# Kernel tuning notes

Measured on AMD Instinct MI355X. Metric: run time of the kernel, lower is better.

## Reference

```python
import jax, jax.numpy as jnp
import numpy as np

GRID = (32, 32)
LATENT = 256
ALPHA = 1.0
DECAY = 0.9


def _cdist(a, b):
    # Euclidean pairwise distance with a grad-safe sqrt (0 where d2==0, like torch.cdist).
    d2 = jnp.sum(a * a, -1)[:, None] + jnp.sum(b * b, -1)[None, :] - 2.0 * (a @ b.T)
    d2 = jnp.maximum(d2, 0.0)
    mask = d2 > 0
    return jnp.where(mask, jnp.sqrt(jnp.where(mask, d2, 1.0)), 0.0)


def setup_inputs() -> dict:
    key = jax.random.key(0)
    k1, k2 = jax.random.split(key)
    z = jax.random.normal(k1, (64, 512, 256), dtype=jnp.float32)
    nodes = jax.random.normal(k2, (GRID[0], GRID[1], LATENT), dtype=jnp.float32)
    return {"z": z, "nodes": nodes}


def reference(z, nodes):
    b, t, d = z.shape
    # time_decay^(seq_len - t - 1)
    tw = DECAY ** (t - 1 - jnp.arange(t, dtype=jnp.float32))
    z_flat = (z * tw[None, :, None]).reshape(b * t, d)   # (b t) d
    nodes_flat = nodes.reshape(-1, d)                     # n d

    dist = _cdist(z_flat, nodes_flat)                     # (b t) n
    q = 1.0 / (1.0 + dist / ALPHA) ** ((ALPHA + 1.0) / 2.0)
    q = q / jnp.sum(q, axis=-1, keepdims=True)            # L1 normalize rows
    q2 = q * q
    p = q2 / jnp.sum(q2, axis=0, keepdims=True)
    p = p / jnp.sum(p, axis=-1, keepdims=True)

    bmu = jnp.argmin(dist, axis=-1).reshape(b, t)         # int32

    # F.kl_div(q.log(), p, reduction='batchmean') = sum(p*(log p - log q)) / N
    kl_loss = jnp.sum(p * (jnp.log(p) - jnp.log(q))) / (b * t)
    diversity_loss = -jnp.mean(_cdist(nodes_flat, nodes_flat))
    time_smooth_loss = jnp.mean((z[:, 1:] - z[:, :-1]) ** 2) * DECAY

    # vectorized neighborhood consistency (python loop in the original is an
    # unweighted mean over all (b, t) adjacent pairs since seq_len is uniform)
    gw = GRID[1]
    pc = jnp.stack([bmu[:, :-1] // gw, bmu[:, :-1] % gw], axis=-1)
    nc = jnp.stack([bmu[:, 1:] // gw, bmu[:, 1:] % gw], axis=-1)
    neighbor_loss = jnp.mean(jnp.sum(jnp.abs(pc - nc), axis=-1).astype(jnp.float32))

    total_loss = kl_loss + 0.5 * diversity_loss + 0.3 * time_smooth_loss + 0.2 * neighbor_loss

    bmu_nodes = nodes_flat[bmu.reshape(-1)].reshape(b, t, d)
    som_z = z + 0.1 * (bmu_nodes - z)
    return (som_z, total_loss, kl_loss, diversity_loss, time_smooth_loss, neighbor_loss, q, bmu)
```

## Files before the change

kernel.cpp:

```cpp
#include <hip/hip_runtime.h>
#include <math.h>

#define Bb 64
#define Tt 512
#define Dd 256
#define Nn 1024
#define NROWS 32768

#define OUT_SOM 0L
#define OUT_SCAL 8388608L
#define OUT_Q 8388613L
#define OUT_BMU 41943045L

typedef __attribute__((ext_vector_type(8))) short bf16x8;
typedef __attribute__((ext_vector_type(4))) float f32x4;
typedef unsigned long long u64;

static __device__ __forceinline__ unsigned short f2bf(float x) {
  unsigned int u = __float_as_uint(x);
  unsigned int r = (u + 0x7fffu + ((u >> 16) & 1u)) >> 16;
  return (unsigned short)r;
}
static __device__ __forceinline__ float bf2f(unsigned short b) {
  return __uint_as_float(((unsigned int)b) << 16);
}

static __device__ __forceinline__ float block_reduce_sum(float v, float* sb) {
#pragma unroll
  for (int o = 32; o > 0; o >>= 1) v += __shfl_down(v, o, 64);
  const int lane = threadIdx.x & 63, w = threadIdx.x >> 6;
  if (lane == 0) sb[w] = v;
  __syncthreads();
  return (threadIdx.x == 0) ? (sb[0] + sb[1] + sb[2] + sb[3]) : 0.0f;
}

__global__ __launch_bounds__(256) void k_convz(const float* __restrict__ z,
                                               unsigned short* __restrict__ zhi,
                                               unsigned short* __restrict__ zlo,
                                               float* __restrict__ zn) {
  const int tid = threadIdx.x, lane = tid & 63, w = tid >> 6;
  const long row = (long)blockIdx.x * 4 + w;
  const int t = (int)(row & (Tt - 1));
  const float tw = powf(0.9f, (float)(Tt - 1 - t));
  const float4 v = ((const float4*)(z + row * Dd))[lane];
  float x[4] = {v.x * tw, v.y * tw, v.z * tw, v.w * tw};
  unsigned short h[4], l[4];
  float s = 0.f;
#pragma unroll
  for (int i = 0; i < 4; ++i) {
    h[i] = f2bf(x[i]);
    l[i] = f2bf(x[i] - bf2f(h[i]));
    s = fmaf(x[i], x[i], s);
  }
  *(ushort4*)(zhi + row * Dd + lane * 4) = make_ushort4(h[0], h[1], h[2], h[3]);
  *(ushort4*)(zlo + row * Dd + lane * 4) = make_ushort4(l[0], l[1], l[2], l[3]);
#pragma unroll
  for (int o = 32; o > 0; o >>= 1) s += __shfl_down(s, o, 64);
  if (lane == 0) zn[row] = s;
}

__global__ __launch_bounds__(256) void k_convn(const float* __restrict__ nodes,
                                               float* __restrict__ nt,
                                               float* __restrict__ nnorm,
                                               unsigned short* __restrict__ nhi,
                                               unsigned short* __restrict__ nlo) {
  __shared__ float sb[4];
  const int j = blockIdx.x, d = threadIdx.x;
  const float v = nodes[j * Dd + d];
  nt[(long)d * Nn + j] = v;
  const unsigned short h = f2bf(v);
  nhi[j * Dd + d] = h;
  nlo[j * Dd + d] = f2bf(v - bf2f(h));
  const float tot = block_reduce_sum(v * v, sb);
  if (threadIdx.x == 0) nnorm[j] = tot;
}

__global__ __launch_bounds__(256) void k_div(const float* __restrict__ nodes,
                                             const float* __restrict__ nt,
                                             const float* __restrict__ nnorm,
                                             float* __restrict__ scal) {
  __shared__ float ni[4][Dd];
  __shared__ float sb[4];
  const int tid = threadIdx.x;
  const int i0 = blockIdx.x * 4;
#pragma unroll
  for (int r = 0; r < 4; ++r) ni[r][tid] = nodes[(i0 + r) * Dd + tid];
  __syncthreads();
  float acc[4][4];
#pragma unroll
  for (int r = 0; r < 4; ++r)
#pragma unroll
    for (int jj = 0; jj < 4; ++jj) acc[r][jj] = 0.f;
  for (int d = 0; d < Dd; ++d) {
    float nj[4];
#pragma unroll
    for (int jj = 0; jj < 4; ++jj) nj[jj] = nt[(long)d * Nn + tid + 256 * jj];
#pragma unroll
    for (int r = 0; r < 4; ++r) {
      const float s = ni[r][d];
#pragma unroll
      for (int jj = 0; jj < 4; ++jj) acc[r][jj] = fmaf(s, nj[jj], acc[r][jj]);
    }
  }
  float sum = 0.f;
#pragma unroll
  for (int r = 0; r < 4; ++r) {
#pragma unroll
    for (int jj = 0; jj < 4; ++jj) {
      const float d2 = nnorm[i0 + r] + nnorm[tid + 256 * jj] - 2.f * acc[r][jj];
      sum += sqrtf(fmaxf(d2, 0.f));
    }
  }
  const float tot = block_reduce_sum(sum, sb);
  if (tid == 0) atomicAdd(&scal[1], tot);
}

__global__ __launch_bounds__(256, 2) void k_gemm(
    const unsigned short* __restrict__ zhi, const unsigned short* __restrict__ zlo,
    const unsigned short* __restrict__ nhi, const unsigned short* __restrict__ nlo,
    const float* __restrict__ zn, const float* __restrict__ nn,
    float* __restrict__ qout, float* __restrict__ part8,
    u64* __restrict__ bmup8) {
  __shared__ __align__(16) unsigned char smem[65536];

  const int tid = threadIdx.x, lane = tid & 63, wave = tid >> 6;
  const int wr = wave >> 1, wc = wave & 1;
  const int rl = lane & 15, kq = lane >> 4;
  const int bm = blockIdx.x & 255, bn = blockIdx.x >> 8;
  const long row0 = (long)bm * 128;
  const int col0 = bn * 128;

  auto stage = [&](int kt, int bufsel) {
    unsigned char* lb = smem + bufsel * 32768;
#pragma unroll
    for (int i = 0; i < 2; ++i) {
      const int rbase = (i * 4 + wave) * 16;
      const int r = rbase + (lane >> 2);
      const int kb = (lane & 3) ^ ((r >> 1) & 3);
      const long ea = (row0 + r) * Dd + kt * 32 + kb * 8;
      const long eb = (long)(col0 + r) * Dd + kt * 32 + kb * 8;
      const int lo = rbase * 64;
      __builtin_amdgcn_global_load_lds(
          (const __attribute__((address_space(1))) void*)(zhi + ea),
          (__attribute__((address_space(3))) void*)(lb + lo), 16, 0, 0);
      __builtin_amdgcn_global_load_lds(
          (const __attribute__((address_space(1))) void*)(zlo + ea),
          (__attribute__((address_space(3))) void*)(lb + 8192 + lo), 16, 0, 0);
      __builtin_amdgcn_global_load_lds(
          (const __attribute__((address_space(1))) void*)(nhi + eb),
          (__attribute__((address_space(3))) void*)(lb + 16384 + lo), 16, 0, 0);
      __builtin_amdgcn_global_load_lds(
          (const __attribute__((address_space(1))) void*)(nlo + eb),
          (__attribute__((address_space(3))) void*)(lb + 24576 + lo), 16, 0, 0);
    }
  };

  f32x4 acc[4][4];
#pragma unroll
  for (int i = 0; i < 4; ++i)
#pragma unroll
    for (int j = 0; j < 4; ++j) acc[i][j] = (f32x4){0.f, 0.f, 0.f, 0.f};

  stage(0, 0);
  __syncthreads();

  const int sx = (kq ^ ((rl >> 1) & 3)) << 4;

  for (int kt = 0; kt < 8; ++kt) {
    if (kt < 7) stage(kt + 1, (kt + 1) & 1);
    unsigned char* lb = smem + (kt & 1) * 32768;
    bf16x8 ah[4], al[4], bh[4], bl[4];
#pragma unroll
    for (int t = 0; t < 4; ++t) {
      const int ra = (wr * 64 + t * 16 + rl) * 64 + sx;
      ah[t] = *(const bf16x8*)(lb + ra);
      al[t] = *(const bf16x8*)(lb + 8192 + ra);
      const int rb = (wc * 64 + t * 16 + rl) * 64 + sx;
      bh[t] = *(const bf16x8*)(lb + 16384 + rb);
      bl[t] = *(const bf16x8*)(lb + 24576 + rb);
    }
#pragma unroll
    for (int i = 0; i < 4; ++i)
#pragma unroll
      for (int j = 0; j < 4; ++j) {
        acc[i][j] = __builtin_amdgcn_mfma_f32_16x16x32_bf16(ah[i], bh[j], acc[i][j], 0, 0, 0);
        acc[i][j] = __builtin_amdgcn_mfma_f32_16x16x32_bf16(ah[i], bl[j], acc[i][j], 0, 0, 0);
        acc[i][j] = __builtin_amdgcn_mfma_f32_16x16x32_bf16(al[i], bh[j], acc[i][j], 0, 0, 0);
      }
    __syncthreads();
  }

  float* srs = (float*)smem;
  u64* sbest = (u64*)(smem + 1024);
  float nnv[4];
#pragma unroll
  for (int j = 0; j < 4; ++j) nnv[j] = nn[col0 + wc * 64 + j * 16 + rl];

#pragma unroll
  for (int i = 0; i < 4; ++i) {
#pragma unroll
    for (int r = 0; r < 4; ++r) {
      const int lrow = wr * 64 + i * 16 + kq * 4 + r;
      const long grow = row0 + lrow;
      const float znv = zn[grow];
      float rs = 0.f;
      u64 best = ~0ull;
#pragma unroll
      for (int j = 0; j < 4; ++j) {
        const float dot = acc[i][j][r];
        const float d2 = znv + nnv[j] - 2.f * dot;
        const float dist = sqrtf(fmaxf(d2, 0.f));
        const float qr = 1.f / (1.f + dist);
        rs += qr;
        const int col = col0 + wc * 64 + j * 16 + rl;
        const u64 pk = ((u64)__float_as_uint(dist) << 32) | (unsigned int)col;
        best = pk < best ? pk : best;
        qout[grow * Nn + col] = qr;
      }
#pragma unroll
      for (int m = 1; m < 16; m <<= 1) {
        rs += __shfl_xor(rs, m, 64);
        const u64 o = __shfl_xor(best, m, 64);
        best = o < best ? o : best;
      }
      if (rl == 0) {
        srs[lrow * 2 + wc] = rs;
        sbest[lrow * 2 + wc] = best;
      }
    }
  }
  __syncthreads();
  if (tid < 128) {
    const long grow = row0 + tid;
    part8[grow * 8 + bn] = srs[tid * 2] + srs[tid * 2 + 1];
    const u64 a = sbest[tid * 2], b = sbest[tid * 2 + 1];
    bmup8[grow * 8 + bn] = a < b ? a : b;
  }
}

__global__ __launch_bounds__(256) void k_unpack(const u64* __restrict__ bmup8,
                                                float* __restrict__ bmuf) {
  const long row = (long)blockIdx.x * 256 + threadIdx.x;
  u64 best = ~0ull;
#pragma unroll
  for (int i = 0; i < 8; ++i) {
    const u64 v = bmup8[row * 8 + i];
    best = v < best ? v : best;
  }
  bmuf[row] = (float)(int)(unsigned int)(best & 0xffffffffull);
}

__global__ __launch_bounds__(256) void k_norm(float* __restrict__ q,
                                              const float* __restrict__ part8,
                                              float* __restrict__ colsum) {
  __shared__ float inv16[16];
  const int tid = threadIdx.x;
  const long r0 = (long)blockIdx.x * 16;
  if (tid < 16) {
    float s = 0.f;
    const float* p = part8 + (r0 + tid) * 8;
#pragma unroll
    for (int i = 0; i < 8; ++i) s += p[i];
    inv16[tid] = 1.f / s;
  }
  __syncthreads();
  float cs[4] = {0.f, 0.f, 0.f, 0.f};
  for (int r = 0; r < 16; ++r) {
    const long row = r0 + r;
    const float inv = inv16[r];
#pragma unroll
    for (int j = 0; j < 4; ++j) {
      const long idx = row * Nn + tid + 256 * j;
      const float v = q[idx] * inv;
      q[idx] = v;
      cs[j] = fmaf(v, v, cs[j]);
    }
  }
#pragma unroll
  for (int j = 0; j < 4; ++j) atomicAdd(&colsum[tid + 256 * j], cs[j]);
}

__global__ __launch_bounds__(256) void k_kl(const float* __restrict__ q,
                                            const float* __restrict__ colsum,
                                            float* __restrict__ scal) {
  __shared__ float csh[Nn];
  __shared__ float sb[4];
  const int tid = threadIdx.x, lane = tid & 63, wave = tid >> 6;
#pragma unroll
  for (int j = 0; j < 4; ++j) csh[tid + 256 * j] = colsum[tid + 256 * j];
  __syncthreads();
  const long r0 = (long)blockIdx.x * 16;
  float klp = 0.f;
  for (int rr = 0; rr < 4; ++rr) {
    const long row = r0 + rr * 4 + wave;
    float qv[16], u[16], s = 0.f;
#pragma unroll
    for (int j = 0; j < 16; ++j) {
      const int col = lane + 64 * j;
      const float t = q[row * Nn + col];
      qv[j] = t;
      const float uu = t * t / csh[col];
      u[j] = uu;
      s += uu;
    }
#pragma unroll
    for (int o = 1; o < 64; o <<= 1) s += __shfl_xor(s, o, 64);
    const float invS = 1.f / s;
#pragma unroll
    for (int j = 0; j < 16; ++j) {
      const float p = u[j] * invS;
      klp += p * (__logf(p) - __logf(qv[j]));
    }
  }
  const float tot = block_reduce_sum(klp, sb);
  if (tid == 0) atomicAdd(&scal[0], tot);
}

__global__ __launch_bounds__(256) void k_som(const float* __restrict__ z,
                                             const float* __restrict__ nodes,
                                             const float* __restrict__ bmuf,
                                             float* __restrict__ som,
                                             float* __restrict__ scal) {
  __shared__ float sb[4];
  const int tid = threadIdx.x;
  const long r0 = (long)blockIdx.x * 16;
  float ts = 0.f, zp = 0.f;
  if ((r0 & (Tt - 1)) > 0) zp = z[(r0 - 1) * Dd + tid];
  for (int r = 0; r < 16; ++r) {
    const long row = r0 + r;
    const float zc = z[row * Dd + tid];
    const int bi = (int)bmuf[row];
    const float nv = nodes[(long)bi * Dd + tid];
    som[row * Dd + tid] = zc + 0.1f * (nv - zc);
    if ((row & (Tt - 1)) > 0) {
      const float dd = zc - zp;
      ts = fmaf(dd, dd, ts);
    }
    zp = zc;
  }
  const float tot = block_reduce_sum(ts, sb);
  if (tid == 0) atomicAdd(&scal[2], tot);
}

__global__ __launch_bounds__(256) void k_nb(const float* __restrict__ bmuf,
                                            float* __restrict__ scal) {
  __shared__ float sb[4];
  const int idx = blockIdx.x * 256 + threadIdx.x;
  float s = 0.f;
  if (idx < Bb * (Tt - 1)) {
    const int b = idx / (Tt - 1);
    const int k = idx - b * (Tt - 1);
    const long row = (long)b * Tt + k;
    const int b1 = (int)bmuf[row], b2 = (int)bmuf[row + 1];
    s = (float)(abs((b1 >> 5) - (b2 >> 5)) + abs((b1 & 31) - (b2 & 31)));
  }
  const float tot = block_reduce_sum(s, sb);
  if (threadIdx.x == 0) atomicAdd(&scal[3], tot);
}

__global__ void k_final(const float* __restrict__ scal, float* __restrict__ o) {
  const float kl = scal[0] * (1.f / 32768.f);
  const float dv = -scal[1] * (1.f / (1024.f * 1024.f));
  const float ts = scal[2] * (0.9f / (64.f * 511.f * 256.f));
  const float nb = scal[3] * (1.f / 32704.f);
  o[0] = kl + 0.5f * dv + 0.3f * ts + 0.2f * nb;
  o[1] = kl;
  o[2] = dv;
  o[3] = ts;
  o[4] = nb;
}

__global__ __launch_bounds__(256) void k_prep_fb(const float* __restrict__ nodes,
                                                 float* __restrict__ nt,
                                                 float* __restrict__ nnorm) {
  __shared__ float sb[4];
  const int j = blockIdx.x, d = threadIdx.x;
  const float v = nodes[j * Dd + d];
  nt[(long)d * Nn + j] = v;
  const float tot = block_reduce_sum(v * v, sb);
  if (threadIdx.x == 0) nnorm[j] = tot;
}

__global__ __launch_bounds__(256) void k_dist_fb(
    const float* __restrict__ z, const float* __restrict__ nt,
    const float* __restrict__ nnorm, float* __restrict__ qout,
    float* __restrict__ srow, float* __restrict__ bmuf) {
  __shared__ float zt[Dd][65];
  __shared__ float rs4[4][64];
  __shared__ u64 cand[4][64];
  const int tid = threadIdx.x, lane = tid & 63, wave = tid >> 6;
  const long row0 = (long)blockIdx.x * 64;
  for (int k = 0; k < 64; ++k) {
    const int t = (int)((row0 + k) & (Tt - 1));
    const float tw = powf(0.9f, (float)(Tt - 1 - t));
    zt[tid][k] = z[(row0 + k) * Dd + tid] * tw;
  }
  __syncthreads();
  float zns = 0.f;
  for (int d = 0; d < Dd; ++d) {
    const float v = zt[d][lane];
    zns = fmaf(v, v, zns);
  }
  const long myrow = row0 + lane;
  float rsum = 0.f;
  u64 best = ~0ull;
  const int j0w = wave * 256;
  for (int chunk = 0; chunk < 16; ++chunk) {
    const int j0 = j0w + chunk * 16;
    float acc[16];
#pragma unroll
    for (int i = 0; i < 16; ++i) acc[i] = 0.f;
    const float* ntp = nt + j0;
    for (int d = 0; d < Dd; ++d) {
      const float zv = zt[d][lane];
      const float4 a = ((const float4*)ntp)[0];
      const float4 b = ((const float4*)ntp)[1];
      const float4 c = ((const float4*)ntp)[2];
      const float4 e = ((const float4*)ntp)[3];
      ntp += Nn;
      acc[0] = fmaf(zv, a.x, acc[0]); acc[1] = fmaf(zv, a.y, acc[1]);
      acc[2] = fmaf(zv, a.z, acc[2]); acc[3] = fmaf(zv, a.w, acc[3]);
      acc[4] = fmaf(zv, b.x, acc[4]); acc[5] = fmaf(zv, b.y, acc[5]);
      acc[6] = fmaf(zv, b.z, acc[6]); acc[7] = fmaf(zv, b.w, acc[7]);
      acc[8] = fmaf(zv, c.x, acc[8]); acc[9] = fmaf(zv, c.y, acc[9]);
      acc[10] = fmaf(zv, c.z, acc[10]); acc[11] = fmaf(zv, c.w, acc[11]);
      acc[12] = fmaf(zv, e.x, acc[12]); acc[13] = fmaf(zv, e.y, acc[13]);
      acc[14] = fmaf(zv, e.z, acc[14]); acc[15] = fmaf(zv, e.w, acc[15]);
    }
#pragma unroll
    for (int jj = 0; jj < 16; ++jj) {
      const int j = j0 + jj;
      const float d2 = zns + nnorm[j] - 2.f * acc[jj];
      const float dist = sqrtf(fmaxf(d2, 0.f));
      const float qr = 1.f / (1.f + dist);
      qout[myrow * Nn + j] = qr;
      rsum += qr;
      const u64 pk = ((u64)__float_as_uint(dist) << 32) | (unsigned int)j;
      best = pk < best ? pk : best;
    }
  }
  rs4[wave][lane] = rsum;
  cand[wave][lane] = best;
  __syncthreads();
  if (wave == 0) {
    const float s = rs4[0][lane] + rs4[1][lane] + rs4[2][lane] + rs4[3][lane];
    srow[myrow] = s;
    const u64 m0 = cand[0][lane] < cand[1][lane] ? cand[0][lane] : cand[1][lane];
    const u64 m1 = cand[2][lane] < cand[3][lane] ? cand[2][lane] : cand[3][lane];
    const u64 m = m0 < m1 ? m0 : m1;
    bmuf[myrow] = (float)(int)(unsigned int)(m & 0xffffffffull);
  }
}

__global__ __launch_bounds__(256) void k_norm_fb(float* __restrict__ q,
                                                 const float* __restrict__ srow,
                                                 float* __restrict__ colsum) {
  const int tid = threadIdx.x;
  const long r0 = (long)blockIdx.x * 16;
  float cs[4] = {0.f, 0.f, 0.f, 0.f};
  for (int r = 0; r < 16; ++r) {
    const long row = r0 + r;
    const float inv = 1.f / srow[row];
#pragma unroll
    for (int j = 0; j < 4; ++j) {
      const long idx = row * Nn + tid + 256 * j;
      const float v = q[idx] * inv;
      q[idx] = v;
      cs[j] = fmaf(v, v, cs[j]);
    }
  }
#pragma unroll
  for (int j = 0; j < 4; ++j) atomicAdd(&colsum[tid + 256 * j], cs[j]);
}

extern "C" void kernel_launch(void* const* d_in, const int* in_sizes, int n_in,
                              void* d_out, int out_size, void* d_ws, size_t ws_size,
                              hipStream_t stream) {
  const float* z = (const float*)d_in[0];
  const float* nodes = (const float*)d_in[1];
  float* out = (float*)d_out;
  unsigned char* ws = (unsigned char*)d_ws;

  float* som = out + OUT_SOM;
  float* scal_out = out + OUT_SCAL;
  float* qout = out + OUT_Q;
  float* bmuf = out + OUT_BMU;

  const size_t NEED = 37888016;
  if (ws_size >= NEED) {
    unsigned short* zhi = (unsigned short*)(ws + 0);
    unsigned short* zlo = (unsigned short*)(ws + 16777216);
    unsigned short* nhi = (unsigned short*)(ws + 33554432);
    unsigned short* nlo = (unsigned short*)(ws + 34078720);
    float* zn = (float*)(ws + 34603008);
    float* ntpart = (float*)(ws + 34734080);
    u64* bmup8 = (u64*)(ws + 35782656);
    float* nnorm = (float*)(ws + 37879808);
    float* colsum = (float*)(ws + 37883904);
    float* scal = (float*)(ws + 37888000);

    hipMemsetAsync(colsum, 0, 4096 + 16, stream);

    k_convz<<<8192, 256, 0, stream>>>(z, zhi, zlo, zn);
    k_convn<<<1024, 256, 0, stream>>>(nodes, ntpart, nnorm, nhi, nlo);
    k_div<<<256, 256, 0, stream>>>(nodes, ntpart, nnorm, scal);
    k_gemm<<<2048, 256, 0, stream>>>(zhi, zlo, nhi, nlo, zn, nnorm, qout, ntpart, bmup8);
    k_unpack<<<128, 256, 0, stream>>>(bmup8, bmuf);
    k_norm<<<2048, 256, 0, stream>>>(qout, ntpart, colsum);
    k_kl<<<2048, 256, 0, stream>>>(qout, colsum, scal);
    k_som<<<2048, 256, 0, stream>>>(z, nodes, bmuf, som, scal);
    k_nb<<<128, 256, 0, stream>>>(bmuf, scal);
    k_final<<<1, 1, 0, stream>>>(scal, scal_out);
  } else {
    float* wsf = (float*)ws;
    float* nt = wsf;
    float* nnorm = wsf + 262144;
    float* srow = wsf + 263168;
    float* colsum = wsf + 295936;
    float* scal = wsf + 296960;

    hipMemsetAsync(colsum, 0, (1024 + 4) * sizeof(float), stream);
    k_prep_fb<<<1024, 256, 0, stream>>>(nodes, nt, nnorm);
    k_div<<<256, 256, 0, stream>>>(nodes, nt, nnorm, scal);
    k_dist_fb<<<512, 256, 0, stream>>>(z, nt, nnorm, qout, srow, bmuf);
    k_norm_fb<<<2048, 256, 0, stream>>>(qout, srow, colsum);
    k_kl<<<2048, 256, 0, stream>>>(qout, colsum, scal);
    k_som<<<2048, 256, 0, stream>>>(z, nodes, bmuf, som, scal);
    k_nb<<<128, 256, 0, stream>>>(bmuf, scal);
    k_final<<<1, 1, 0, stream>>>(scal, scal_out);
  }
}
```

Baseline: 298.0 us.

## Interleave hi/lo bf16 operands, fuse conversions, MFMA diversity, vectorize norm/KL, merge som+nb

Stores the hi and lo bf16 parts of z and nodes side by side in one row of 512 elements. The split-bf16 GEMM now runs as a single K=768 loop with one MFMA per step and a smaller LDS footprint, with no launch-bounds occupancy hint. The z and node conversion kernels are merged into one launch. The node-node diversity term now uses MFMA on the split bf16 data instead of a scalar FP32 loop. The norm and KL kernels switch to float4 access, and KL precomputes reciprocal and log column sums, rewriting the per-row term as a/s - log s. The neighbor loss is folded into the som kernel. Together these remove several launches and extra FP32 work, at the risk of small accuracy differences in the diversity and KL terms.

```diff
diff --git a/kernel.cpp b/kernel.cpp
--- a/kernel.cpp
+++ b/kernel.cpp
@@ -15,6 +15,7 @@
 typedef __attribute__((ext_vector_type(8))) short bf16x8;
 typedef __attribute__((ext_vector_type(4))) float f32x4;
 typedef unsigned long long u64;
+typedef unsigned short ushortT;
 
 static __device__ __forceinline__ unsigned short f2bf(float x) {
   unsigned int u = __float_as_uint(x);
@@ -34,95 +35,50 @@
   return (threadIdx.x == 0) ? (sb[0] + sb[1] + sb[2] + sb[3]) : 0.0f;
 }
 
-__global__ __launch_bounds__(256) void k_convz(const float* __restrict__ z,
-                                               unsigned short* __restrict__ zhi,
-                                               unsigned short* __restrict__ zlo,
-                                               float* __restrict__ zn) {
+__global__ __launch_bounds__(256) void k_conv2(
+    const float* __restrict__ z, const float* __restrict__ nodes,
+    ushortT* __restrict__ A2, ushortT* __restrict__ B2,
+    float* __restrict__ zn, float* __restrict__ nnorm) {
   const int tid = threadIdx.x, lane = tid & 63, w = tid >> 6;
-  const long row = (long)blockIdx.x * 4 + w;
-  const int t = (int)(row & (Tt - 1));
-  const float tw = powf(0.9f, (float)(Tt - 1 - t));
-  const float4 v = ((const float4*)(z + row * Dd))[lane];
-  float x[4] = {v.x * tw, v.y * tw, v.z * tw, v.w * tw};
-  unsigned short h[4], l[4];
-  float s = 0.f;
-#pragma unroll
-  for (int i = 0; i < 4; ++i) {
-    h[i] = f2bf(x[i]);
-    l[i] = f2bf(x[i] - bf2f(h[i]));
-    s = fmaf(x[i], x[i], s);
-  }
-  *(ushort4*)(zhi + row * Dd + lane * 4) = make_ushort4(h[0], h[1], h[2], h[3]);
-  *(ushort4*)(zlo + row * Dd + lane * 4) = make_ushort4(l[0], l[1], l[2], l[3]);
-#pragma unroll
-  for (int o = 32; o > 0; o >>= 1) s += __shfl_down(s, o, 64);
-  if (lane == 0) zn[row] = s;
-}
-
-__global__ __launch_bounds__(256) void k_convn(const float* __restrict__ nodes,
-                                               float* __restrict__ nt,
-                                               float* __restrict__ nnorm,
-                                               unsigned short* __restrict__ nhi,
-                                               unsigned short* __restrict__ nlo) {
-  __shared__ float sb[4];
-  const int j = blockIdx.x, d = threadIdx.x;
-  const float v = nodes[j * Dd + d];
-  nt[(long)d * Nn + j] = v;
-  const unsigned short h = f2bf(v);
-  nhi[j * Dd + d] = h;
-  nlo[j * Dd + d] = f2bf(v - bf2f(h));
-  const float tot = block_reduce_sum(v * v, sb);
-  if (threadIdx.x == 0) nnorm[j] = tot;
-}
-
-__global__ __launch_bounds__(256) void k_div(const float* __restrict__ nodes,
-                                             const float* __restrict__ nt,
-                                             const float* __restrict__ nnorm,
-                                             float* __restrict__ scal) {
-  __shared__ float ni[4][Dd];
-  __shared__ float sb[4];
-  const int tid = threadIdx.x;
-  const int i0 = blockIdx.x * 4;
-#pragma unroll
-  for (int r = 0; r < 4; ++r) ni[r][tid] = nodes[(i0 + r) * Dd + tid];
-  __syncthreads();
-  float acc[4][4];
-#pragma unroll
-  for (int r = 0; r < 4; ++r)
-#pragma unroll
-    for (int jj = 0; jj < 4; ++jj) acc[r][jj] = 0.f;
-  for (int d = 0; d < Dd; ++d) {
-    float nj[4];
-#pragma unroll
-    for (int jj = 0; jj < 4; ++jj) nj[jj] = nt[(long)d * Nn + tid + 256 * jj];
-#pragma unroll
-    for (int r = 0; r < 4; ++r) {
-      const float s = ni[r][d];
-#pragma unroll
-      for (int jj = 0; jj < 4; ++jj) acc[r][jj] = fmaf(s, nj[jj], acc[r][jj]);
-    }
-  }
-  float sum = 0.f;
-#pragma unroll
-  for (int r = 0; r < 4; ++r) {
-#pragma unroll
-    for (int jj = 0; jj < 4; ++jj) {
-      const float d2 = nnorm[i0 + r] + nnorm[tid + 256 * jj] - 2.f * acc[r][jj];
-      sum += sqrtf(fmaxf(d2, 0.f));
-    }
-  }
-  const float tot = block_reduce_sum(sum, sb);
-  if (tid == 0) atomicAdd(&scal[1], tot);
-}
-
-__global__ __launch_bounds__(256, 2) void k_gemm(
-    const unsigned short* __restrict__ zhi, const unsigned short* __restrict__ zlo,
-    const unsigned short* __restrict__ nhi, const unsigned short* __restrict__ nlo,
+  if (blockIdx.x < 8192) {
+    const long row = (long)blockIdx.x * 4 + w;
+    const int t = (int)(row & (Tt - 1));
+    const float tw = powf(0.9f, (float)(Tt - 1 - t));
+    const float4 v = ((const float4*)(z + row * Dd))[lane];
+    float x0 = v.x * tw, x1 = v.y * tw, x2 = v.z * tw, x3 = v.w * tw;
+    ushort4 h, l;
+    h.x = f2bf(x0); l.x = f2bf(x0 - bf2f(h.x));
+    h.y = f2bf(x1); l.y = f2bf(x1 - bf2f(h.y));
+    h.z = f2bf(x2); l.z = f2bf(x2 - bf2f(h.z));
+    h.w = f2bf(x3); l.w = f2bf(x3 - bf2f(h.w));
+    *(ushort4*)(A2 + row * 512 + lane * 4) = h;
+    *(ushort4*)(A2 + row * 512 + 256 + lane * 4) = l;
+    float s = x0 * x0 + x1 * x1 + x2 * x2 + x3 * x3;
+#pragma unroll
+    for (int o = 32; o > 0; o >>= 1) s += __shfl_down(s, o, 64);
+    if (lane == 0) zn[row] = s;
+  } else {
+    const long j = (long)(blockIdx.x - 8192) * 4 + w;
+    const float4 v = ((const float4*)(nodes + j * Dd))[lane];
+    ushort4 h, l;
+    h.x = f2bf(v.x); l.x = f2bf(v.x - bf2f(h.x));
+    h.y = f2bf(v.y); l.y = f2bf(v.y - bf2f(h.y));
+    h.z = f2bf(v.z); l.z = f2bf(v.z - bf2f(h.z));
+    h.w = f2bf(v.w); l.w = f2bf(v.w - bf2f(h.w));
+    *(ushort4*)(B2 + j * 512 + lane * 4) = h;
+    *(ushort4*)(B2 + j * 512 + 256 + lane * 4) = l;
+    float s = v.x * v.x + v.y * v.y + v.z * v.z + v.w * v.w;
+#pragma unroll
+    for (int o = 32; o > 0; o >>= 1) s += __shfl_down(s, o, 64);
+    if (lane == 0) nnorm[j] = s;
+  }
+}
+
+__global__ __launch_bounds__(256) void k_gemm6(
+    const ushortT* __restrict__ A2, const ushortT* __restrict__ B2,
     const float* __restrict__ zn, const float* __restrict__ nn,
-    float* __restrict__ qout, float* __restrict__ part8,
-    u64* __restrict__ bmup8) {
-  __shared__ __align__(16) unsigned char smem[65536];
-
+    float* __restrict__ qout, float* __restrict__ part8, u64* __restrict__ bmup8) {
+  __shared__ __align__(16) unsigned char smem[32768];
   const int tid = threadIdx.x, lane = tid & 63, wave = tid >> 6;
   const int wr = wave >> 1, wc = wave & 1;
   const int rl = lane & 15, kq = lane >> 4;
@@ -131,27 +87,23 @@
   const int col0 = bn * 128;
 
   auto stage = [&](int kt, int bufsel) {
-    unsigned char* lb = smem + bufsel * 32768;
+    unsigned char* lb = smem + bufsel * 16384;
+    const int koffA = kt < 8 ? kt * 32 : (kt < 16 ? (kt - 8) * 32 : 256 + (kt - 16) * 32);
+    const int koffB = kt < 8 ? kt * 32 : (kt < 16 ? 256 + (kt - 8) * 32 : (kt - 16) * 32);
 #pragma unroll
     for (int i = 0; i < 2; ++i) {
       const int rbase = (i * 4 + wave) * 16;
       const int r = rbase + (lane >> 2);
       const int kb = (lane & 3) ^ ((r >> 1) & 3);
-      const long ea = (row0 + r) * Dd + kt * 32 + kb * 8;
-      const long eb = (long)(col0 + r) * Dd + kt * 32 + kb * 8;
+      const long ea = (row0 + r) * 512 + koffA + kb * 8;
+      const long eb = (long)(col0 + r) * 512 + koffB + kb * 8;
       const int lo = rbase * 64;
       __builtin_amdgcn_global_load_lds(
-          (const __attribute__((address_space(1))) void*)(zhi + ea),
+          (const __attribute__((address_space(1))) void*)(A2 + ea),
           (__attribute__((address_space(3))) void*)(lb + lo), 16, 0, 0);
       __builtin_amdgcn_global_load_lds(
-          (const __attribute__((address_space(1))) void*)(zlo + ea),
+          (const __attribute__((address_space(1))) void*)(B2 + eb),
           (__attribute__((address_space(3))) void*)(lb + 8192 + lo), 16, 0, 0);
-      __builtin_amdgcn_global_load_lds(
-          (const __attribute__((address_space(1))) void*)(nhi + eb),
-          (__attribute__((address_space(3))) void*)(lb + 16384 + lo), 16, 0, 0);
-      __builtin_amdgcn_global_load_lds(
-          (const __attribute__((address_space(1))) void*)(nlo + eb),
-          (__attribute__((address_space(3))) void*)(lb + 24576 + lo), 16, 0, 0);
     }
   };
 
@@ -166,27 +118,20 @@
 
   const int sx = (kq ^ ((rl >> 1) & 3)) << 4;
 
-  for (int kt = 0; kt < 8; ++kt) {
-    if (kt < 7) stage(kt + 1, (kt + 1) & 1);
-    unsigned char* lb = smem + (kt & 1) * 32768;
-    bf16x8 ah[4], al[4], bh[4], bl[4];
+  for (int kt = 0; kt < 24; ++kt) {
+    if (kt < 23) stage(kt + 1, (kt + 1) & 1);
+    unsigned char* lb = smem + (kt & 1) * 16384;
+    bf16x8 a[4], b[4];
 #pragma unroll
     for (int t = 0; t < 4; ++t) {
-      const int ra = (wr * 64 + t * 16 + rl) * 64 + sx;
-      ah[t] = *(const bf16x8*)(lb + ra);
-      al[t] = *(const bf16x8*)(lb + 8192 + ra);
-      const int rb = (wc * 64 + t * 16 + rl) * 64 + sx;
-      bh[t] = *(const bf16x8*)(lb + 16384 + rb);
-      bl[t] = *(const bf16x8*)(lb + 24576 + rb);
+      a[t] = *(const bf16x8*)(lb + (wr * 64 + t * 16 + rl) * 64 + sx);
+      b[t] = *(const bf16x8*)(lb + 8192 + (wc * 64 + t * 16 + rl) * 64 + sx);
     }
 #pragma unroll
     for (int i = 0; i < 4; ++i)
 #pragma unroll
-      for (int j = 0; j < 4; ++j) {
-        acc[i][j] = __builtin_amdgcn_mfma_f32_16x16x32_bf16(ah[i], bh[j], acc[i][j], 0, 0, 0);
-        acc[i][j] = __builtin_amdgcn_mfma_f32_16x16x32_bf16(ah[i], bl[j], acc[i][j], 0, 0, 0);
-        acc[i][j] = __builtin_amdgcn_mfma_f32_16x16x32_bf16(al[i], bh[j], acc[i][j], 0, 0, 0);
-      }
+      for (int j = 0; j < 4; ++j)
+        acc[i][j] = __builtin_amdgcn_mfma_f32_16x16x32_bf16(a[i], b[j], acc[i][j], 0, 0, 0);
     __syncthreads();
   }
 
@@ -233,8 +178,8 @@
   if (tid < 128) {
     const long grow = row0 + tid;
     part8[grow * 8 + bn] = srs[tid * 2] + srs[tid * 2 + 1];
-    const u64 a = sbest[tid * 2], b = sbest[tid * 2 + 1];
-    bmup8[grow * 8 + bn] = a < b ? a : b;
+    const u64 a0 = sbest[tid * 2], b0 = sbest[tid * 2 + 1];
+    bmup8[grow * 8 + bn] = a0 < b0 ? a0 : b0;
   }
 }
 
@@ -264,63 +209,117 @@
     inv16[tid] = 1.f / s;
   }
   __syncthreads();
-  float cs[4] = {0.f, 0.f, 0.f, 0.f};
+  float cs0 = 0.f, cs1 = 0.f, cs2 = 0.f, cs3 = 0.f;
   for (int r = 0; r < 16; ++r) {
     const long row = r0 + r;
     const float inv = inv16[r];
-#pragma unroll
-    for (int j = 0; j < 4; ++j) {
-      const long idx = row * Nn + tid + 256 * j;
-      const float v = q[idx] * inv;
-      q[idx] = v;
-      cs[j] = fmaf(v, v, cs[j]);
-    }
-  }
-#pragma unroll
-  for (int j = 0; j < 4; ++j) atomicAdd(&colsum[tid + 256 * j], cs[j]);
+    float4 v = *(const float4*)(q + row * Nn + tid * 4);
+    v.x *= inv; v.y *= inv; v.z *= inv; v.w *= inv;
+    *(float4*)(q + row * Nn + tid * 4) = v;
+    cs0 = fmaf(v.x, v.x, cs0);
+    cs1 = fmaf(v.y, v.y, cs1);
+    cs2 = fmaf(v.z, v.z, cs2);
+    cs3 = fmaf(v.w, v.w, cs3);
+  }
+  atomicAdd(&colsum[tid * 4 + 0], cs0);
+  atomicAdd(&colsum[tid * 4 + 1], cs1);
+  atomicAdd(&colsum[tid * 4 + 2], cs2);
+  atomicAdd(&colsum[tid * 4 + 3], cs3);
+}
+
+__global__ __launch_bounds__(256) void k_div3(const ushortT* __restrict__ B2,
+                                              const float* __restrict__ nnorm,
+                                              float* __restrict__ scal) {
+  __shared__ float sb[4];
+  const int tid = threadIdx.x, lane = tid & 63, w = tid >> 6;
+  const int rl = lane & 15, kq = lane >> 4;
+  const int bi = blockIdx.x & 63;
+  const int cq = blockIdx.x >> 6;
+  const ushortT* Abase = B2 + (long)(bi * 16 + rl) * 512 + kq * 8;
+
+  f32x4 acc[4];
+#pragma unroll
+  for (int c = 0; c < 4; ++c) acc[c] = (f32x4){0.f, 0.f, 0.f, 0.f};
+
+#pragma unroll 1
+  for (int ks = 0; ks < 24; ++ks) {
+    const int koffA = ks < 8 ? ks * 32 : (ks < 16 ? (ks - 8) * 32 : 256 + (ks - 16) * 32);
+    const int koffB = ks < 8 ? ks * 32 : (ks < 16 ? 256 + (ks - 8) * 32 : (ks - 16) * 32);
+    const bf16x8 a = *(const bf16x8*)(Abase + koffA);
+#pragma unroll
+    for (int c = 0; c < 4; ++c) {
+      const int ct = cq * 16 + w * 4 + c;
+      const bf16x8 b = *(const bf16x8*)(B2 + (long)(ct * 16 + rl) * 512 + koffB + kq * 8);
+      acc[c] = __builtin_amdgcn_mfma_f32_16x16x32_bf16(a, b, acc[c], 0, 0, 0);
+    }
+  }
+  float ni[4];
+#pragma unroll
+  for (int r = 0; r < 4; ++r) ni[r] = nnorm[bi * 16 + kq * 4 + r];
+  float dsum = 0.f;
+#pragma unroll
+  for (int c = 0; c < 4; ++c) {
+    const int ct = cq * 16 + w * 4 + c;
+    const float nj = nnorm[ct * 16 + rl];
+#pragma unroll
+    for (int r = 0; r < 4; ++r) {
+      const float d2 = ni[r] + nj - 2.f * acc[c][r];
+      dsum += sqrtf(fmaxf(d2, 0.f));
+    }
+  }
+  const float tot = block_reduce_sum(dsum, sb);
+  if (tid == 0) atomicAdd(&scal[1], tot);
 }
 
 __global__ __launch_bounds__(256) void k_kl(const float* __restrict__ q,
                                             const float* __restrict__ colsum,
                                             float* __restrict__ scal) {
-  __shared__ float csh[Nn];
+  __shared__ float4 rcs4[Nn / 4];
+  __shared__ float4 lcs4[Nn / 4];
   __shared__ float sb[4];
   const int tid = threadIdx.x, lane = tid & 63, wave = tid >> 6;
-#pragma unroll
-  for (int j = 0; j < 4; ++j) csh[tid + 256 * j] = colsum[tid + 256 * j];
+  {
+    const float c0 = colsum[tid * 4 + 0];
+    const float c1 = colsum[tid * 4 + 1];
+    const float c2 = colsum[tid * 4 + 2];
+    const float c3 = colsum[tid * 4 + 3];
+    rcs4[tid] = make_float4(1.f / c0, 1.f / c1, 1.f / c2, 1.f / c3);
+    lcs4[tid] = make_float4(__logf(c0), __logf(c1), __logf(c2), __logf(c3));
+  }
   __syncthreads();
   const long r0 = (long)blockIdx.x * 16;
   float klp = 0.f;
   for (int rr = 0; rr < 4; ++rr) {
     const long row = r0 + rr * 4 + wave;
-    float qv[16], u[16], s = 0.f;
-#pragma unroll
-    for (int j = 0; j < 16; ++j) {
-      const int col = lane + 64 * j;
-      const float t = q[row * Nn + col];
-      qv[j] = t;
-      const float uu = t * t / csh[col];
-      u[j] = uu;
-      s += uu;
-    }
-#pragma unroll
-    for (int o = 1; o < 64; o <<= 1) s += __shfl_xor(s, o, 64);
-    const float invS = 1.f / s;
-#pragma unroll
-    for (int j = 0; j < 16; ++j) {
-      const float p = u[j] * invS;
-      klp += p * (__logf(p) - __logf(qv[j]));
-    }
+    float s = 0.f, a = 0.f;
+#pragma unroll
+    for (int j = 0; j < 4; ++j) {
+      const int c4 = lane + 64 * j;
+      const float4 qv = *(const float4*)(q + row * Nn + c4 * 4);
+      const float4 rc = rcs4[c4];
+      const float4 lc = lcs4[c4];
+      float u;
+      u = qv.x * qv.x * rc.x; s += u; a = fmaf(u, __logf(qv.x) - lc.x, a);
+      u = qv.y * qv.y * rc.y; s += u; a = fmaf(u, __logf(qv.y) - lc.y, a);
+      u = qv.z * qv.z * rc.z; s += u; a = fmaf(u, __logf(qv.z) - lc.z, a);
+      u = qv.w * qv.w * rc.w; s += u; a = fmaf(u, __logf(qv.w) - lc.w, a);
+    }
+#pragma unroll
+    for (int o = 1; o < 64; o <<= 1) {
+      s += __shfl_xor(s, o, 64);
+      a += __shfl_xor(a, o, 64);
+    }
+    if (lane == 0) klp += a / s - __logf(s);
   }
   const float tot = block_reduce_sum(klp, sb);
   if (tid == 0) atomicAdd(&scal[0], tot);
 }
 
-__global__ __launch_bounds__(256) void k_som(const float* __restrict__ z,
-                                             const float* __restrict__ nodes,
-                                             const float* __restrict__ bmuf,
-                                             float* __restrict__ som,
-                                             float* __restrict__ scal) {
+__global__ __launch_bounds__(256) void k_somnb(const float* __restrict__ z,
+                                               const float* __restrict__ nodes,
+                                               const float* __restrict__ bmuf,
+                                               float* __restrict__ som,
+                                               float* __restrict__ scal) {
   __shared__ float sb[4];
   const int tid = threadIdx.x;
   const long r0 = (long)blockIdx.x * 16;
@@ -338,24 +337,19 @@
     }
     zp = zc;
   }
-  const float tot = block_reduce_sum(ts, sb);
-  if (tid == 0) atomicAdd(&scal[2], tot);
-}
-
-__global__ __launch_bounds__(256) void k_nb(const float* __restrict__ bmuf,
-                                            float* __restrict__ scal) {
-  __shared__ float sb[4];
-  const int idx = blockIdx.x * 256 + threadIdx.x;
-  float s = 0.f;
-  if (idx < Bb * (Tt - 1)) {
-    const int b = idx / (Tt - 1);
-    const int k = idx - b * (Tt - 1);
-    const long row = (long)b * Tt + k;
-    const int b1 = (int)bmuf[row], b2 = (int)bmuf[row + 1];
-    s = (float)(abs((b1 >> 5) - (b2 >> 5)) + abs((b1 & 31) - (b2 & 31)));
-  }
-  const float tot = block_reduce_sum(s, sb);
-  if (threadIdx.x == 0) atomicAdd(&scal[3], tot);
+  const float tts = block_reduce_sum(ts, sb);
+  if (tid == 0) atomicAdd(&scal[2], tts);
+  float nbv = 0.f;
+  if (tid < 16) {
+    const long row = r0 + tid;
+    if ((row & (Tt - 1)) != (Tt - 1)) {
+      const int b1 = (int)bmuf[row], b2 = (int)bmuf[row + 1];
+      nbv = (float)(abs((b1 >> 5) - (b2 >> 5)) + abs((b1 & 31) - (b2 & 31)));
+    }
+  }
+  __syncthreads();
+  const float tnb = block_reduce_sum(nbv, sb);
+  if (tid == 0) atomicAdd(&scal[3], tnb);
 }
 
 __global__ void k_final(const float* __restrict__ scal, float* __restrict__ o) {
@@ -379,6 +373,45 @@
   nt[(long)d * Nn + j] = v;
   const float tot = block_reduce_sum(v * v, sb);
   if (threadIdx.x == 0) nnorm[j] = tot;
+}
+
+__global__ __launch_bounds__(256) void k_div_fb(const float* __restrict__ nodes,
+                                                const float* __restrict__ nt,
+                                                const float* __restrict__ nnorm,
+                                                float* __restrict__ scal) {
+  __shared__ float ni[4][Dd];
+  __shared__ float sb[4];
+  const int tid = threadIdx.x;
+  const int i0 = blockIdx.x * 4;
+#pragma unroll
+  for (int r = 0; r < 4; ++r) ni[r][tid] = nodes[(i0 + r) * Dd + tid];
+  __syncthreads();
+  float acc[4][4];
+#pragma unroll
+  for (int r = 0; r < 4; ++r)
+#pragma unroll
+    for (int jj = 0; jj < 4; ++jj) acc[r][jj] = 0.f;
+  for (int d = 0; d < Dd; ++d) {
+    float nj[4];
+#pragma unroll
+    for (int jj = 0; jj < 4; ++jj) nj[jj] = nt[(long)d * Nn + tid + 256 * jj];
+#pragma unroll
+    for (int r = 0; r < 4; ++r) {
+      const float s = ni[r][d];
+#pragma unroll
+      for (int jj = 0; jj < 4; ++jj) acc[r][jj] = fmaf(s, nj[jj], acc[r][jj]);
+    }
+  }
+  float sum = 0.f;
+#pragma unroll
+  for (int r = 0; r < 4; ++r)
+#pragma unroll
+    for (int jj = 0; jj < 4; ++jj) {
+      const float d2 = nnorm[i0 + r] + nnorm[tid + 256 * jj] - 2.f * acc[r][jj];
+      sum += sqrtf(fmaxf(d2, 0.f));
+    }
+  const float tot = block_reduce_sum(sum, sb);
+  if (tid == 0) atomicAdd(&scal[1], tot);
 }
 
 __global__ __launch_bounds__(256) void k_dist_fb(
@@ -488,28 +521,24 @@
 
   const size_t NEED = 37888016;
   if (ws_size >= NEED) {
-    unsigned short* zhi = (unsigned short*)(ws + 0);
-    unsigned short* zlo = (unsigned short*)(ws + 16777216);
-    unsigned short* nhi = (unsigned short*)(ws + 33554432);
-    unsigned short* nlo = (unsigned short*)(ws + 34078720);
+    ushortT* A2 = (ushortT*)(ws + 0);
+    ushortT* B2 = (ushortT*)(ws + 33554432);
     float* zn = (float*)(ws + 34603008);
-    float* ntpart = (float*)(ws + 34734080);
-    u64* bmup8 = (u64*)(ws + 35782656);
-    float* nnorm = (float*)(ws + 37879808);
+    float* nnorm = (float*)(ws + 34734080);
+    float* part8 = (float*)(ws + 34738176);
+    u64* bmup8 = (u64*)(ws + 35786752);
     float* colsum = (float*)(ws + 37883904);
     float* scal = (float*)(ws + 37888000);
 
     hipMemsetAsync(colsum, 0, 4096 + 16, stream);
 
-    k_convz<<<8192, 256, 0, stream>>>(z, zhi, zlo, zn);
-    k_convn<<<1024, 256, 0, stream>>>(nodes, ntpart, nnorm, nhi, nlo);
-    k_div<<<256, 256, 0, stream>>>(nodes, ntpart, nnorm, scal);
-    k_gemm<<<2048, 256, 0, stream>>>(zhi, zlo, nhi, nlo, zn, nnorm, qout, ntpart, bmup8);
+    k_conv2<<<8448, 256, 0, stream>>>(z, nodes, A2, B2, zn, nnorm);
+    k_gemm6<<<2048, 256, 0, stream>>>(A2, B2, zn, nnorm, qout, part8, bmup8);
     k_unpack<<<128, 256, 0, stream>>>(bmup8, bmuf);
-    k_norm<<<2048, 256, 0, stream>>>(qout, ntpart, colsum);
+    k_norm<<<2048, 256, 0, stream>>>(qout, part8, colsum);
+    k_div3<<<256, 256, 0, stream>>>(B2, nnorm, scal);
     k_kl<<<2048, 256, 0, stream>>>(qout, colsum, scal);
-    k_som<<<2048, 256, 0, stream>>>(z, nodes, bmuf, som, scal);
-    k_nb<<<128, 256, 0, stream>>>(bmuf, scal);
+    k_somnb<<<2048, 256, 0, stream>>>(z, nodes, bmuf, som, scal);
     k_final<<<1, 1, 0, stream>>>(scal, scal_out);
   } else {
     float* wsf = (float*)ws;
@@ -521,12 +550,11 @@
 
     hipMemsetAsync(colsum, 0, (1024 + 4) * sizeof(float), stream);
     k_prep_fb<<<1024, 256, 0, stream>>>(nodes, nt, nnorm);
-    k_div<<<256, 256, 0, stream>>>(nodes, nt, nnorm, scal);
+    k_div_fb<<<256, 256, 0, stream>>>(nodes, nt, nnorm, scal);
     k_dist_fb<<<512, 256, 0, stream>>>(z, nt, nnorm, qout, srow, bmuf);
     k_norm_fb<<<2048, 256, 0, stream>>>(qout, srow, colsum);
     k_kl<<<2048, 256, 0, stream>>>(qout, colsum, scal);
-    k_som<<<2048, 256, 0, stream>>>(z, nodes, bmuf, som, scal);
-    k_nb<<<128, 256, 0, stream>>>(bmuf, scal);
+    k_somnb<<<2048, 256, 0, stream>>>(z, nodes, bmuf, som, scal);
     k_final<<<1, 1, 0, stream>>>(scal, scal_out);
   }
 }
```

Measured after the change: 465.9 us. 56.3% more time.
